# Kernel optimization log

Hardware: AMD Instinct MI355X
Metric: run time of the kernel (lower is better)

## Reference

```python
import jax, jax.numpy as jnp
import numpy as np

EMBED_DIM = 1024
WINDOW = 256
NUM_HEADS = 16
HEAD_DIM = EMBED_DIM // NUM_HEADS
SCALE = HEAD_DIM ** (-0.5)


def setup_inputs() -> dict:
    key = jax.random.key(0)
    ks = jax.random.split(key, 9)
    B, S, E = 4, 4096, EMBED_DIM
    std = E ** (-0.5)
    x = jax.random.normal(ks[0], (B, S, E), dtype=jnp.float32)
    Wq = jax.random.normal(ks[1], (E, E), dtype=jnp.float32) * std
    Wk = jax.random.normal(ks[2], (E, E), dtype=jnp.float32) * std
    Wv = jax.random.normal(ks[3], (E, E), dtype=jnp.float32) * std
    Wo = jax.random.normal(ks[4], (E, E), dtype=jnp.float32) * std
    bq = jax.random.normal(ks[5], (E,), dtype=jnp.float32) * 0.01
    bk = jax.random.normal(ks[6], (E,), dtype=jnp.float32) * 0.01
    bv = jax.random.normal(ks[7], (E,), dtype=jnp.float32) * 0.01
    bo = jax.random.normal(ks[8], (E,), dtype=jnp.float32) * 0.01
    return {"x": x, "Wq": Wq, "bq": bq, "Wk": Wk, "bk": bk,
            "Wv": Wv, "bv": bv, "Wo": Wo, "bo": bo}


def reference(x, Wq, bq, Wk, bk, Wv, bv, Wo, bo):
    B, S, E = x.shape
    W = WINDOW
    nw = S // W  # seq_len chosen divisible by window_size
    # projections (torch Linear: x @ W.T + b); no head split in the original
    q = x @ Wq.T + bq
    k = x @ Wk.T + bk
    v = x @ Wv.T + bv
    # split into non-overlapping windows: [B, nw, W, E]
    qw = q.reshape(B, nw, W, E)
    kw = k.reshape(B, nw, W, E)
    vw = v.reshape(B, nw, W, E)
    scores = jnp.einsum('bnqe,bnke->bnqk', qw, kw) * SCALE  # [B, nw, W, W]
    causal = jnp.tril(jnp.ones((W, W), dtype=bool))
    scores = jnp.where(causal, scores, -jnp.inf)
    attn = jax.nn.softmax(scores, axis=-1)
    out = jnp.einsum('bnqk,bnke->bnqe', attn, vw).reshape(B, S, E)
    out = out @ Wo.T + bo
    return out + x
```

## Files before the change

### kernel.cpp

```cpp
#include <hip/hip_runtime.h>
#include <hip/hip_bf16.h>


typedef unsigned short u16;
typedef __attribute__((ext_vector_type(8))) short short8;
typedef __attribute__((ext_vector_type(4))) short short4v;
typedef __attribute__((ext_vector_type(4))) float f32x4;

__device__ __forceinline__ u16 f2bf(float f) {
    __hip_bfloat16 h = __float2bfloat16(f);
    return __builtin_bit_cast(u16, h);
}

__global__ void cast_f32_bf16(const float* __restrict__ src, u16* __restrict__ dst, int n) {
    int i = (blockIdx.x * 256 + threadIdx.x) * 8;
    if (i >= n) return;
    const float4* s = (const float4*)(src + i);
    float4 a = s[0], b = s[1];
    short8 o;
    o[0] = (short)f2bf(a.x); o[1] = (short)f2bf(a.y); o[2] = (short)f2bf(a.z); o[3] = (short)f2bf(a.w);
    o[4] = (short)f2bf(b.x); o[5] = (short)f2bf(b.y); o[6] = (short)f2bf(b.z); o[7] = (short)f2bf(b.w);
    *(short8*)(dst + i) = o;
}

__global__ void wcast(const float* __restrict__ Wq, const float* __restrict__ Wk,
                      const float* __restrict__ Wv, const float* __restrict__ Wo,
                      u16* __restrict__ WqT, u16* __restrict__ WkT,
                      u16* __restrict__ WvT, u16* __restrict__ Wob)
{
    __shared__ float lt[64][65];
    const int which = blockIdx.x >> 8;
    const int bid = blockIdx.x & 255;
    const int c0 = (bid & 15) * 64, r0 = (bid >> 4) * 64;
    const int t = threadIdx.x;
    const int tr = t >> 3, tc = (t & 7) * 8;
    const float* src = which == 0 ? Wq : which == 1 ? Wk : which == 2 ? Wv : Wo;
    if (which == 3) {
#pragma unroll
        for (int p = 0; p < 2; ++p) {
            int r = p * 32 + tr;
            const float* s = src + (size_t)(r0 + r) * 1024 + c0 + tc;
            float4 a = *(const float4*)s, b = *(const float4*)(s + 4);
            short8 o;
            o[0] = (short)f2bf(a.x); o[1] = (short)f2bf(a.y); o[2] = (short)f2bf(a.z); o[3] = (short)f2bf(a.w);
            o[4] = (short)f2bf(b.x); o[5] = (short)f2bf(b.y); o[6] = (short)f2bf(b.z); o[7] = (short)f2bf(b.w);
            *(short8*)(Wob + (size_t)(r0 + r) * 1024 + c0 + tc) = o;
        }
        return;
    }
    u16* dst = which == 0 ? WqT : which == 1 ? WkT : WvT;
#pragma unroll
    for (int p = 0; p < 2; ++p) {
        int r = p * 32 + tr;
        const float* s = src + (size_t)(r0 + r) * 1024 + c0 + tc;
        float4 a = *(const float4*)s, b = *(const float4*)(s + 4);
        lt[r][tc + 0] = a.x; lt[r][tc + 1] = a.y; lt[r][tc + 2] = a.z; lt[r][tc + 3] = a.w;
        lt[r][tc + 4] = b.x; lt[r][tc + 5] = b.y; lt[r][tc + 6] = b.z; lt[r][tc + 7] = b.w;
    }
    __syncthreads();
#pragma unroll
    for (int p = 0; p < 2; ++p) {
        int r = p * 32 + tr;
        short8 o;
#pragma unroll
        for (int j = 0; j < 8; ++j) o[j] = (short)f2bf(lt[tc + j][r]);
        *(short8*)(dst + (size_t)(c0 + r) * 1024 + r0 + tc) = o;
    }
}

__global__ void ub2(const float* __restrict__ Wk, const float* __restrict__ bq,
                    const float* __restrict__ Wo, const float* __restrict__ bv,
                    const float* __restrict__ bo, float* __restrict__ u, float* __restrict__ b2)
{
    const int t = threadIdx.x, bid = blockIdx.x;
    if (bid < 4) {
        int b = bid * 256 + t;
        float acc = 0.f;
        for (int o = 0; o < 1024; ++o) acc += Wk[(size_t)o * 1024 + b] * bq[o];
        u[b] = acc;
    } else {
        int n = (bid - 4) * 16 + (t >> 4);
        int l = t & 15;
        float acc = 0.f;
        for (int m = l; m < 1024; m += 16) acc += Wo[(size_t)n * 1024 + m] * bv[m];
#pragma unroll
        for (int s = 1; s < 16; s <<= 1) acc += __shfl_xor(acc, s, 64);
        if (l == 0) b2[n] = acc + bo[n];
    }
}

__global__ __launch_bounds__(256, 4) void gemm_small_dual(
    const u16* __restrict__ HA, const u16* __restrict__ HB, u16* __restrict__ HC,
    const u16* __restrict__ WA, const u16* __restrict__ WB, u16* __restrict__ WC)
{
    __shared__ __align__(16) u16 At[64 * 64], Bt[64 * 64];
    const bool sec = blockIdx.x >= 256;
    const u16* A = sec ? WA : HA;
    const u16* B = sec ? WB : HB;
    u16* C = sec ? WC : HC;
    const int bid = blockIdx.x & 255;
    const int m0 = (bid >> 4) * 64, n0 = (bid & 15) * 64;
    const int t = threadIdx.x, lane = t & 63, w = t >> 6;
    const int l15 = lane & 15, lk = lane >> 4;

    f32x4 acc[4];
#pragma unroll
    for (int m = 0; m < 4; ++m) acc[m] = (f32x4){0.f, 0.f, 0.f, 0.f};

    for (int k0 = 0; k0 < 1024; k0 += 64) {
        __syncthreads();
#pragma unroll
        for (int p = 0; p < 2; ++p) {
            int e = p * 2048 + t * 8;
            int row = e >> 6, col = e & 63;
            short8 va = *(const short8*)(A + (size_t)(m0 + row) * 1024 + k0 + col);
            *(short8*)((char*)At + row * 128 + ((col * 2) ^ ((row & 7) << 4))) = va;
            short8 vb = *(const short8*)(B + (size_t)(n0 + row) * 1024 + k0 + col);
            *(short8*)((char*)Bt + row * 128 + ((col * 2) ^ ((row & 7) << 4))) = vb;
        }
        __syncthreads();
#pragma unroll
        for (int ks = 0; ks < 2; ++ks) {
            int bc = ks * 64 + lk * 16;
            int brow = w * 16 + l15;
            short8 bfr = *(const short8*)((char*)Bt + brow * 128 + (bc ^ ((brow & 7) << 4)));
#pragma unroll
            for (int m = 0; m < 4; ++m) {
                int arow = m * 16 + l15;
                short8 af = *(const short8*)((char*)At + arow * 128 + (bc ^ ((arow & 7) << 4)));
                acc[m] = __builtin_amdgcn_mfma_f32_16x16x32_bf16(af, bfr, acc[m], 0, 0, 0);
            }
        }
    }
#pragma unroll
    for (int m = 0; m < 4; ++m)
#pragma unroll
        for (int r = 0; r < 4; ++r) {
            int row = m0 + m * 16 + lk * 4 + r;
            int col = n0 + w * 16 + l15;
            C[(size_t)row * 1024 + col] = f2bf(acc[m][r]);
        }
}

__global__ __launch_bounds__(256, 2) void gemm_yv(
    const u16* __restrict__ A, const u16* __restrict__ BH, const u16* __restrict__ BW,
    const float* __restrict__ ub, u16* __restrict__ Y, u16* __restrict__ V2t)
{
    __shared__ __align__(16) char smbuf[2 * 32768];
    const int t = threadIdx.x;
    const int lane = t & 63;
    const int wid = t >> 6;
    const int wm = wid >> 1, wn = wid & 1;
    const int l15 = lane & 15, lk = lane >> 4;
    const int K = 1024;

    const int bid = blockIdx.y * gridDim.x + blockIdx.x;
    const int cpx = 2048 >> 3;
    const int swz = (bid & 7) * cpx + (bid >> 3);
    const int tn = swz & 15;
    const int tm = swz >> 4;
    const int m0 = tm * 128;
    const bool isv = tn >= 8;
    const int n0 = (tn & 7) * 128;
    const u16* B = isv ? BW : BH;

    const int srow = (t * 8) >> 6, scol = (t * 8) & 63;

    f32x4 acc[4][4];
#pragma unroll
    for (int m = 0; m < 4; ++m)
#pragma unroll
        for (int n = 0; n < 4; ++n)
            acc[m][n] = (f32x4){0.f, 0.f, 0.f, 0.f};

    short8 pva[4], pvb[4];
    auto LOAD = [&](int k0) {
#pragma unroll
        for (int p = 0; p < 4; ++p) {
            int row = p * 32 + srow;
            pva[p] = *(const short8*)(A + (size_t)(m0 + row) * K + k0 + scol);
            pvb[p] = *(const short8*)(B + (size_t)(n0 + row) * K + k0 + scol);
        }
    };
    auto WRITE = [&](int b) {
        char* At = smbuf + b * 32768;
        char* Bt = At + 16384;
#pragma unroll
        for (int p = 0; p < 4; ++p) {
            int row = p * 32 + srow;
            *(short8*)(At + row * 128 + ((scol * 2) ^ ((row & 7) << 4))) = pva[p];
            *(short8*)(Bt + row * 128 + ((scol * 2) ^ ((row & 7) << 4))) = pvb[p];
        }
    };

    LOAD(0);
    WRITE(0);
    LOAD(64);
    __syncthreads();

    for (int i = 0; i < 16; ++i) {
        const int b = i & 1;
        if (i + 1 < 16) {
            WRITE(b ^ 1);
            if (i + 2 < 16) LOAD((i + 2) * 64);
        }
        const char* At = smbuf + b * 32768;
        const char* Bt = At + 16384;
#pragma unroll
        for (int ks = 0; ks < 2; ++ks) {
            const int bc = ks * 64 + lk * 16;
            short8 af[4], bfr[4];
#pragma unroll
            for (int m = 0; m < 4; ++m) {
                int row = wm * 64 + m * 16 + l15;
                af[m] = *(const short8*)(At + row * 128 + (bc ^ ((row & 7) << 4)));
            }
#pragma unroll
            for (int n = 0; n < 4; ++n) {
                int row = wn * 64 + n * 16 + l15;
                bfr[n] = *(const short8*)(Bt + row * 128 + (bc ^ ((row & 7) << 4)));
            }
            __builtin_amdgcn_s_setprio(1);
#pragma unroll
            for (int m = 0; m < 4; ++m)
#pragma unroll
                for (int n = 0; n < 4; ++n)
                    acc[m][n] = __builtin_amdgcn_mfma_f32_16x16x32_bf16(af[m], bfr[n], acc[m][n], 0, 0, 0);
            __builtin_amdgcn_s_setprio(0);
        }
        __syncthreads();
    }

    if (!isv) {
#pragma unroll
        for (int m = 0; m < 4; ++m)
#pragma unroll
            for (int n = 0; n < 4; ++n) {
                int col = n0 + wn * 64 + n * 16 + l15;
                float bv = ub[col];
#pragma unroll
                for (int r = 0; r < 4; ++r) {
                    int row = m0 + wm * 64 + m * 16 + lk * 4 + r;
                    Y[(size_t)row * 1024 + col] = f2bf(acc[m][n][r] + bv);
                }
            }
    } else {
#pragma unroll
        for (int m = 0; m < 4; ++m)
#pragma unroll
            for (int n = 0; n < 4; ++n) {
                int col = n0 + wn * 64 + n * 16 + l15;
                int row0 = m0 + wm * 64 + m * 16 + lk * 4;
                short4v pk;
#pragma unroll
                for (int r = 0; r < 4; ++r) pk[r] = (short)f2bf(acc[m][n][r]);
                *(short4v*)(V2t + (size_t)col * 16384 + row0) = pk;
            }
    }
}

__global__ __launch_bounds__(256, 1) void attn_win(
    const u16* __restrict__ y, const u16* __restrict__ xb,
    const u16* __restrict__ vt, const float* __restrict__ xres,
    const float* __restrict__ b2, float* __restrict__ outp)
{
    __shared__ __align__(16) char smem[116736];
    u16* P  = (u16*)(smem + 81920);
    float* rmax = (float*)(smem + 114688);
    float* rsum = (float*)(smem + 115712);

    const int t = threadIdx.x;
    const int lane = t & 63, wv = t >> 6;
    const int l15 = lane & 15, lk = lane >> 4;
    const int bid = blockIdx.x;
    const int swz = (bid & 7) * 32 + (bid >> 3);
    const int win = swz >> 2, qc = swz & 3;
    const size_t qrow0 = (size_t)win * 256 + qc * 64;
    const size_t krow0 = (size_t)win * 256;

    f32x4 acc[4][4];
#pragma unroll
    for (int m = 0; m < 4; ++m)
#pragma unroll
        for (int n = 0; n < 4; ++n)
            acc[m][n] = (f32x4){0.f, 0.f, 0.f, 0.f};

    short8 pq[2], pk[8];
    auto LOAD_QK = [&](int e0) {
#pragma unroll
        for (int p = 0; p < 2; ++p) {
            int e = p * 2048 + t * 8;
            pq[p] = *(const short8*)(y + (qrow0 + (e >> 6)) * 1024 + e0 + (e & 63));
        }
#pragma unroll
        for (int p = 0; p < 8; ++p) {
            int e = p * 2048 + t * 8;
            pk[p] = *(const short8*)(xb + (krow0 + (e >> 6)) * 1024 + e0 + (e & 63));
        }
    };
    auto WRITE_QK = [&](int b) {
        char* Qt = smem + b * 40960;
        char* Kt = Qt + 8192;
#pragma unroll
        for (int p = 0; p < 2; ++p) {
            int e = p * 2048 + t * 8;
            int row = e >> 6, col = e & 63;
            *(short8*)(Qt + row * 128 + ((col * 2) ^ ((row & 7) << 4))) = pq[p];
        }
#pragma unroll
        for (int p = 0; p < 8; ++p) {
            int e = p * 2048 + t * 8;
            int row = e >> 6, col = e & 63;
            *(short8*)(Kt + row * 128 + ((col * 2) ^ ((row & 7) << 4))) = pk[p];
        }
    };

    LOAD_QK(0);
    WRITE_QK(0);
    LOAD_QK(64);
    __syncthreads();

    for (int i = 0; i < 16; ++i) {
        const int b = i & 1;
        if (i + 1 < 16) {
            WRITE_QK(b ^ 1);
            if (i + 2 < 16) LOAD_QK((i + 2) * 64);
        }
        const char* Qt = smem + b * 40960;
        const char* Kt = Qt + 8192;
#pragma unroll
        for (int ks = 0; ks < 2; ++ks) {
            const int bc = ks * 64 + lk * 16;
            short8 af[4], bfr[4];
#pragma unroll
            for (int m = 0; m < 4; ++m) {
                int row = m * 16 + l15;
                af[m] = *(const short8*)(Qt + row * 128 + (bc ^ ((row & 7) << 4)));
            }
#pragma unroll
            for (int n = 0; n < 4; ++n) {
                int row = wv * 64 + n * 16 + l15;
                bfr[n] = *(const short8*)(Kt + row * 128 + (bc ^ ((row & 7) << 4)));
            }
            __builtin_amdgcn_s_setprio(1);
#pragma unroll
            for (int m = 0; m < 4; ++m)
#pragma unroll
                for (int n = 0; n < 4; ++n)
                    acc[m][n] = __builtin_amdgcn_mfma_f32_16x16x32_bf16(af[m], bfr[n], acc[m][n], 0, 0, 0);
            __builtin_amdgcn_s_setprio(0);
        }
        __syncthreads();
    }

#pragma unroll
    for (int m = 0; m < 4; ++m)
#pragma unroll
        for (int n = 0; n < 4; ++n) {
            int col = wv * 64 + n * 16 + l15;
#pragma unroll
            for (int r = 0; r < 4; ++r) {
                int qpos = qc * 64 + m * 16 + lk * 4 + r;
                float v = acc[m][n][r] * 0.125f;
                acc[m][n][r] = (col <= qpos) ? v : -1e30f;
            }
        }
#pragma unroll
    for (int m = 0; m < 4; ++m)
#pragma unroll
        for (int r = 0; r < 4; ++r) {
            float tmx = fmaxf(fmaxf(acc[m][0][r], acc[m][1][r]), fmaxf(acc[m][2][r], acc[m][3][r]));
            tmx = fmaxf(tmx, __shfl_xor(tmx, 1));
            tmx = fmaxf(tmx, __shfl_xor(tmx, 2));
            tmx = fmaxf(tmx, __shfl_xor(tmx, 4));
            tmx = fmaxf(tmx, __shfl_xor(tmx, 8));
            if (l15 == 0) rmax[(m * 16 + lk * 4 + r) * 4 + wv] = tmx;
        }
    __syncthreads();
#pragma unroll
    for (int m = 0; m < 4; ++m)
#pragma unroll
        for (int r = 0; r < 4; ++r) {
            int row = m * 16 + lk * 4 + r;
            float m4 = fmaxf(fmaxf(rmax[row * 4], rmax[row * 4 + 1]),
                             fmaxf(rmax[row * 4 + 2], rmax[row * 4 + 3]));
            float s = 0.f;
#pragma unroll
            for (int n = 0; n < 4; ++n) {
                float e = __expf(acc[m][n][r] - m4);
                acc[m][n][r] = e;
                s += e;
            }
            s += __shfl_xor(s, 1);
            s += __shfl_xor(s, 2);
            s += __shfl_xor(s, 4);
            s += __shfl_xor(s, 8);
            if (l15 == 0) rsum[row * 4 + wv] = s;
        }
    __syncthreads();
#pragma unroll
    for (int m = 0; m < 4; ++m)
#pragma unroll
        for (int r = 0; r < 4; ++r) {
            int row = m * 16 + lk * 4 + r;
            float inv = 1.f / (rsum[row * 4] + rsum[row * 4 + 1] + rsum[row * 4 + 2] + rsum[row * 4 + 3]);
#pragma unroll
            for (int n = 0; n < 4; ++n) {
                int col = wv * 64 + n * 16 + l15;
                *(u16*)((char*)P + row * 512 + ((col * 2) ^ ((row & 7) << 4))) = f2bf(acc[m][n][r] * inv);
            }
        }

    short8 pv[8];
    auto LOAD_V = [&](int n0) {
#pragma unroll
        for (int p = 0; p < 8; ++p) {
            int e = p * 2048 + t * 8;
            pv[p] = *(const short8*)(vt + (size_t)(n0 + (e >> 8)) * 16384 + win * 256 + (e & 255));
        }
    };
    auto WRITE_V = [&](int b) {
        char* Vl = smem + b * 40960;
#pragma unroll
        for (int p = 0; p < 8; ++p) {
            int e = p * 2048 + t * 8;
            int row = e >> 8, col = e & 255;
            *(short8*)(Vl + row * 512 + ((col * 2) ^ ((row & 7) << 4))) = pv[p];
        }
    };

    LOAD_V(0);
    WRITE_V(0);
    LOAD_V(64);
    __syncthreads();

    for (int i = 0; i < 16; ++i) {
        const int b = i & 1;
        const int n0 = i * 64;
        if (i + 1 < 16) {
            WRITE_V(b ^ 1);
            if (i + 2 < 16) LOAD_V((i + 2) * 64);
        }
        const char* Vl = smem + b * 40960;
        f32x4 acc2[4];
#pragma unroll
        for (int m = 0; m < 4; ++m) acc2[m] = (f32x4){0.f, 0.f, 0.f, 0.f};
#pragma unroll
        for (int ks = 0; ks < 8; ++ks) {
            const int bc = ks * 64 + lk * 16;
            short8 af[4];
#pragma unroll
            for (int m = 0; m < 4; ++m) {
                int row = m * 16 + l15;
                af[m] = *(const short8*)((char*)P + row * 512 + (bc ^ ((row & 7) << 4)));
            }
            int vrow = wv * 16 + l15;
            short8 bfr = *(const short8*)(Vl + vrow * 512 + (bc ^ ((vrow & 7) << 4)));
            __builtin_amdgcn_s_setprio(1);
#pragma unroll
            for (int m = 0; m < 4; ++m)
                acc2[m] = __builtin_amdgcn_mfma_f32_16x16x32_bf16(af[m], bfr, acc2[m], 0, 0, 0);
            __builtin_amdgcn_s_setprio(0);
        }
#pragma unroll
        for (int m = 0; m < 4; ++m) {
#pragma unroll
            for (int r = 0; r < 4; ++r) {
                int row = m * 16 + lk * 4 + r;
                int col = n0 + wv * 16 + l15;
                size_t idx = (qrow0 + row) * 1024 + col;
                outp[idx] = acc2[m][r] + b2[col] + xres[idx];
            }
        }
        __syncthreads();
    }
}

extern "C" void kernel_launch(void* const* d_in, const int* in_sizes, int n_in,
                              void* d_out, int out_size, void* d_ws, size_t ws_size,
                              hipStream_t stream) {
    const float* x  = (const float*)d_in[0];
    const float* Wq = (const float*)d_in[1];
    const float* bq = (const float*)d_in[2];
    const float* Wk = (const float*)d_in[3];
    const float* Wv = (const float*)d_in[5];
    const float* bv = (const float*)d_in[6];
    const float* Wo = (const float*)d_in[7];
    const float* bo = (const float*)d_in[8];
    float* out = (float*)d_out;

    char* ws = (char*)d_ws;
    u16* xb  = (u16*)(ws);
    u16* yb  = (u16*)(ws + 33554432);
    u16* v2t = (u16*)(ws + 67108864);
    u16* WqT = (u16*)(ws + 100663296);
    u16* WkT = (u16*)(ws + 102760448);
    u16* WvT = (u16*)(ws + 104857600);
    u16* Wob = (u16*)(ws + 106954752);
    u16* Hb  = (u16*)(ws + 109051904);
    u16* W2b = (u16*)(ws + 111149056);
    float* u_  = (float*)(ws + 113246208);
    float* b2_ = (float*)(ws + 113250304);

    cast_f32_bf16<<<8192, 256, 0, stream>>>(x, xb, 16777216);
    wcast<<<1024, 256, 0, stream>>>(Wq, Wk, Wv, Wo, WqT, WkT, WvT, Wob);
    ub2<<<68, 256, 0, stream>>>(Wk, bq, Wo, bv, bo, u_, b2_);
    gemm_small_dual<<<512, 256, 0, stream>>>(WkT, WqT, Hb, Wob, WvT, W2b);
    gemm_yv<<<dim3(16, 128), 256, 0, stream>>>(xb, Hb, W2b, u_, yb, v2t);
    attn_win<<<256, 256, 0, stream>>>(yb, xb, v2t, x, b2_, out);
}
```

Before: 196.5 us.

## Merge prep kernels into one launch and halve GEMM K-tile to 32

Result: no change. 197.0 us (+0.2%).

```diff
diff --git a/kernel.cpp b/kernel.cpp
--- a/kernel.cpp
+++ b/kernel.cpp
@@ -12,80 +12,84 @@
     return __builtin_bit_cast(u16, h);
 }
 
-__global__ void cast_f32_bf16(const float* __restrict__ src, u16* __restrict__ dst, int n) {
-    int i = (blockIdx.x * 256 + threadIdx.x) * 8;
-    if (i >= n) return;
-    const float4* s = (const float4*)(src + i);
-    float4 a = s[0], b = s[1];
-    short8 o;
-    o[0] = (short)f2bf(a.x); o[1] = (short)f2bf(a.y); o[2] = (short)f2bf(a.z); o[3] = (short)f2bf(a.w);
-    o[4] = (short)f2bf(b.x); o[5] = (short)f2bf(b.y); o[6] = (short)f2bf(b.z); o[7] = (short)f2bf(b.w);
-    *(short8*)(dst + i) = o;
-}
-
-__global__ void wcast(const float* __restrict__ Wq, const float* __restrict__ Wk,
-                      const float* __restrict__ Wv, const float* __restrict__ Wo,
-                      u16* __restrict__ WqT, u16* __restrict__ WkT,
-                      u16* __restrict__ WvT, u16* __restrict__ Wob)
+__global__ void prep(const float* __restrict__ x, u16* __restrict__ xb,
+                     const float* __restrict__ Wq, const float* __restrict__ Wk,
+                     const float* __restrict__ Wv, const float* __restrict__ Wo,
+                     u16* __restrict__ WqT, u16* __restrict__ WkT,
+                     u16* __restrict__ WvT, u16* __restrict__ Wob,
+                     const float* __restrict__ bq, const float* __restrict__ bv,
+                     const float* __restrict__ bo,
+                     float* __restrict__ u, float* __restrict__ b2)
 {
     __shared__ float lt[64][65];
-    const int which = blockIdx.x >> 8;
-    const int bid = blockIdx.x & 255;
-    const int c0 = (bid & 15) * 64, r0 = (bid >> 4) * 64;
     const int t = threadIdx.x;
-    const int tr = t >> 3, tc = (t & 7) * 8;
-    const float* src = which == 0 ? Wq : which == 1 ? Wk : which == 2 ? Wv : Wo;
-    if (which == 3) {
+    const int blk = blockIdx.x;
+    if (blk < 8192) {
+        int i = (blk * 256 + t) * 8;
+        const float4* s = (const float4*)(x + i);
+        float4 a = s[0], b = s[1];
+        short8 o;
+        o[0] = (short)f2bf(a.x); o[1] = (short)f2bf(a.y); o[2] = (short)f2bf(a.z); o[3] = (short)f2bf(a.w);
+        o[4] = (short)f2bf(b.x); o[5] = (short)f2bf(b.y); o[6] = (short)f2bf(b.z); o[7] = (short)f2bf(b.w);
+        *(short8*)(xb + i) = o;
+        return;
+    }
+    if (blk < 9216) {
+        const int wb = blk - 8192;
+        const int which = wb >> 8;
+        const int bid = wb & 255;
+        const int c0 = (bid & 15) * 64, r0 = (bid >> 4) * 64;
+        const int tr = t >> 3, tc = (t & 7) * 8;
+        const float* src = which == 0 ? Wq : which == 1 ? Wk : which == 2 ? Wv : Wo;
+        if (which == 3) {
+#pragma unroll
+            for (int p = 0; p < 2; ++p) {
+                int r = p * 32 + tr;
+                const float* s = src + (size_t)(r0 + r) * 1024 + c0 + tc;
+                float4 a = *(const float4*)s, b = *(const float4*)(s + 4);
+                short8 o;
+                o[0] = (short)f2bf(a.x); o[1] = (short)f2bf(a.y); o[2] = (short)f2bf(a.z); o[3] = (short)f2bf(a.w);
+                o[4] = (short)f2bf(b.x); o[5] = (short)f2bf(b.y); o[6] = (short)f2bf(b.z); o[7] = (short)f2bf(b.w);
+                *(short8*)(Wob + (size_t)(r0 + r) * 1024 + c0 + tc) = o;
+            }
+            return;
+        }
+        u16* dst = which == 0 ? WqT : which == 1 ? WkT : WvT;
 #pragma unroll
         for (int p = 0; p < 2; ++p) {
             int r = p * 32 + tr;
             const float* s = src + (size_t)(r0 + r) * 1024 + c0 + tc;
             float4 a = *(const float4*)s, b = *(const float4*)(s + 4);
+            lt[r][tc + 0] = a.x; lt[r][tc + 1] = a.y; lt[r][tc + 2] = a.z; lt[r][tc + 3] = a.w;
+            lt[r][tc + 4] = b.x; lt[r][tc + 5] = b.y; lt[r][tc + 6] = b.z; lt[r][tc + 7] = b.w;
+        }
+        __syncthreads();
+#pragma unroll
+        for (int p = 0; p < 2; ++p) {
+            int r = p * 32 + tr;
             short8 o;
-            o[0] = (short)f2bf(a.x); o[1] = (short)f2bf(a.y); o[2] = (short)f2bf(a.z); o[3] = (short)f2bf(a.w);
-            o[4] = (short)f2bf(b.x); o[5] = (short)f2bf(b.y); o[6] = (short)f2bf(b.z); o[7] = (short)f2bf(b.w);
-            *(short8*)(Wob + (size_t)(r0 + r) * 1024 + c0 + tc) = o;
+#pragma unroll
+            for (int j = 0; j < 8; ++j) o[j] = (short)f2bf(lt[tc + j][r]);
+            *(short8*)(dst + (size_t)(c0 + r) * 1024 + r0 + tc) = o;
         }
         return;
     }
-    u16* dst = which == 0 ? WqT : which == 1 ? WkT : WvT;
-#pragma unroll
-    for (int p = 0; p < 2; ++p) {
-        int r = p * 32 + tr;
-        const float* s = src + (size_t)(r0 + r) * 1024 + c0 + tc;
-        float4 a = *(const float4*)s, b = *(const float4*)(s + 4);
-        lt[r][tc + 0] = a.x; lt[r][tc + 1] = a.y; lt[r][tc + 2] = a.z; lt[r][tc + 3] = a.w;
-        lt[r][tc + 4] = b.x; lt[r][tc + 5] = b.y; lt[r][tc + 6] = b.z; lt[r][tc + 7] = b.w;
-    }
-    __syncthreads();
-#pragma unroll
-    for (int p = 0; p < 2; ++p) {
-        int r = p * 32 + tr;
-        short8 o;
-#pragma unroll
-        for (int j = 0; j < 8; ++j) o[j] = (short)f2bf(lt[tc + j][r]);
-        *(short8*)(dst + (size_t)(c0 + r) * 1024 + r0 + tc) = o;
-    }
-}
-
-__global__ void ub2(const float* __restrict__ Wk, const float* __restrict__ bq,
-                    const float* __restrict__ Wo, const float* __restrict__ bv,
-                    const float* __restrict__ bo, float* __restrict__ u, float* __restrict__ b2)
-{
-    const int t = threadIdx.x, bid = blockIdx.x;
-    if (bid < 4) {
-        int b = bid * 256 + t;
-        float acc = 0.f;
-        for (int o = 0; o < 1024; ++o) acc += Wk[(size_t)o * 1024 + b] * bq[o];
-        u[b] = acc;
-    } else {
-        int n = (bid - 4) * 16 + (t >> 4);
-        int l = t & 15;
-        float acc = 0.f;
-        for (int m = l; m < 1024; m += 16) acc += Wo[(size_t)n * 1024 + m] * bv[m];
-#pragma unroll
-        for (int s = 1; s < 16; s <<= 1) acc += __shfl_xor(acc, s, 64);
-        if (l == 0) b2[n] = acc + bo[n];
+    {
+        const int bid = blk - 9216;
+        if (bid < 4) {
+            int b = bid * 256 + t;
+            float acc = 0.f;
+            for (int o = 0; o < 1024; ++o) acc += Wk[(size_t)o * 1024 + b] * bq[o];
+            u[b] = acc;
+        } else {
+            int n = (bid - 4) * 16 + (t >> 4);
+            int l = t & 15;
+            float acc = 0.f;
+            for (int m = l; m < 1024; m += 16) acc += Wo[(size_t)n * 1024 + m] * bv[m];
+#pragma unroll
+            for (int s = 1; s < 16; s <<= 1) acc += __shfl_xor(acc, s, 64);
+            if (l == 0) b2[n] = acc + bo[n];
+        }
     }
 }
 
@@ -146,7 +150,7 @@
     const u16* __restrict__ A, const u16* __restrict__ BH, const u16* __restrict__ BW,
     const float* __restrict__ ub, u16* __restrict__ Y, u16* __restrict__ V2t)
 {
-    __shared__ __align__(16) char smbuf[2 * 32768];
+    __shared__ __align__(16) char smbuf[2 * 16384];
     const int t = threadIdx.x;
     const int lane = t & 63;
     const int wid = t >> 6;
@@ -164,7 +168,7 @@
     const int n0 = (tn & 7) * 128;
     const u16* B = isv ? BW : BH;
 
-    const int srow = (t * 8) >> 6, scol = (t * 8) & 63;
+    const int srow = t >> 2, scol = (t & 3) * 8;
 
     f32x4 acc[4][4];
 #pragma unroll
@@ -173,61 +177,57 @@
         for (int n = 0; n < 4; ++n)
             acc[m][n] = (f32x4){0.f, 0.f, 0.f, 0.f};
 
-    short8 pva[4], pvb[4];
+    short8 pva[2], pvb[2];
     auto LOAD = [&](int k0) {
 #pragma unroll
-        for (int p = 0; p < 4; ++p) {
-            int row = p * 32 + srow;
+        for (int p = 0; p < 2; ++p) {
+            int row = p * 64 + srow;
             pva[p] = *(const short8*)(A + (size_t)(m0 + row) * K + k0 + scol);
             pvb[p] = *(const short8*)(B + (size_t)(n0 + row) * K + k0 + scol);
         }
     };
     auto WRITE = [&](int b) {
-        char* At = smbuf + b * 32768;
-        char* Bt = At + 16384;
-#pragma unroll
-        for (int p = 0; p < 4; ++p) {
-            int row = p * 32 + srow;
-            *(short8*)(At + row * 128 + ((scol * 2) ^ ((row & 7) << 4))) = pva[p];
-            *(short8*)(Bt + row * 128 + ((scol * 2) ^ ((row & 7) << 4))) = pvb[p];
+        char* At = smbuf + b * 16384;
+        char* Bt = At + 8192;
+#pragma unroll
+        for (int p = 0; p < 2; ++p) {
+            int row = p * 64 + srow;
+            *(short8*)(At + row * 64 + ((scol * 2) ^ ((row & 3) << 4))) = pva[p];
+            *(short8*)(Bt + row * 64 + ((scol * 2) ^ ((row & 3) << 4))) = pvb[p];
         }
     };
 
     LOAD(0);
     WRITE(0);
-    LOAD(64);
+    LOAD(32);
     __syncthreads();
 
-    for (int i = 0; i < 16; ++i) {
+    for (int i = 0; i < 32; ++i) {
         const int b = i & 1;
-        if (i + 1 < 16) {
+        if (i + 1 < 32) {
             WRITE(b ^ 1);
-            if (i + 2 < 16) LOAD((i + 2) * 64);
-        }
-        const char* At = smbuf + b * 32768;
-        const char* Bt = At + 16384;
-#pragma unroll
-        for (int ks = 0; ks < 2; ++ks) {
-            const int bc = ks * 64 + lk * 16;
-            short8 af[4], bfr[4];
-#pragma unroll
-            for (int m = 0; m < 4; ++m) {
-                int row = wm * 64 + m * 16 + l15;
-                af[m] = *(const short8*)(At + row * 128 + (bc ^ ((row & 7) << 4)));
-            }
-#pragma unroll
-            for (int n = 0; n < 4; ++n) {
-                int row = wn * 64 + n * 16 + l15;
-                bfr[n] = *(const short8*)(Bt + row * 128 + (bc ^ ((row & 7) << 4)));
-            }
-            __builtin_amdgcn_s_setprio(1);
-#pragma unroll
-            for (int m = 0; m < 4; ++m)
-#pragma unroll
-                for (int n = 0; n < 4; ++n)
-                    acc[m][n] = __builtin_amdgcn_mfma_f32_16x16x32_bf16(af[m], bfr[n], acc[m][n], 0, 0, 0);
-            __builtin_amdgcn_s_setprio(0);
-        }
+            if (i + 2 < 32) LOAD((i + 2) * 32);
+        }
+        const char* At = smbuf + b * 16384;
+        const char* Bt = At + 8192;
+        short8 af[4], bfr[4];
+#pragma unroll
+        for (int m = 0; m < 4; ++m) {
+            int row = wm * 64 + m * 16 + l15;
+            af[m] = *(const short8*)(At + row * 64 + ((lk * 16) ^ ((row & 3) << 4)));
+        }
+#pragma unroll
+        for (int n = 0; n < 4; ++n) {
+            int row = wn * 64 + n * 16 + l15;
+            bfr[n] = *(const short8*)(Bt + row * 64 + ((lk * 16) ^ ((row & 3) << 4)));
+        }
+        __builtin_amdgcn_s_setprio(1);
+#pragma unroll
+        for (int m = 0; m < 4; ++m)
+#pragma unroll
+            for (int n = 0; n < 4; ++n)
+                acc[m][n] = __builtin_amdgcn_mfma_f32_16x16x32_bf16(af[m], bfr[n], acc[m][n], 0, 0, 0);
+        __builtin_amdgcn_s_setprio(0);
         __syncthreads();
     }
 
@@ -502,9 +502,8 @@
     float* u_  = (float*)(ws + 113246208);
     float* b2_ = (float*)(ws + 113250304);
 
-    cast_f32_bf16<<<8192, 256, 0, stream>>>(x, xb, 16777216);
-    wcast<<<1024, 256, 0, stream>>>(Wq, Wk, Wv, Wo, WqT, WkT, WvT, Wob);
-    ub2<<<68, 256, 0, stream>>>(Wk, bq, Wo, bv, bo, u_, b2_);
+    prep<<<9284, 256, 0, stream>>>(x, xb, Wq, Wk, Wv, Wo, WqT, WkT, WvT, Wob,
+                                   bq, bv, bo, u_, b2_);
     gemm_small_dual<<<512, 256, 0, stream>>>(WkT, WqT, Hb, Wob, WvT, W2b);
     gemm_yv<<<dim3(16, 128), 256, 0, stream>>>(xb, Hb, W2b, u_, yb, v2t);
     attn_win<<<256, 256, 0, stream>>>(yb, xb, v2t, x, b2_, out);
```
